# Kernel tuning notes

Hardware: AMD Instinct MI355X
Metric: run time of the kernel (lower is better)

The kernel has to match this reference:

```python
import jax, jax.numpy as jnp
import numpy as np

B, S, D, H = 2, 2048, 1024, 16
DK = D // H


def setup_inputs() -> dict:
    key = jax.random.key(0)
    ks = jax.random.split(key, 12)
    scale = 1.0 / np.sqrt(D)
    return {
        "query": jax.random.normal(ks[0], (B, S, D), jnp.float32),
        "key": jax.random.normal(ks[1], (B, S, D), jnp.float32),
        "value": jax.random.normal(ks[2], (B, S, D), jnp.float32),
        "mask": jax.random.randint(ks[3], (B, S), 0, 2, jnp.int32),
        "Wq": jax.random.normal(ks[4], (D, D), jnp.float32) * scale,
        "bq": jnp.zeros((D,), jnp.float32),
        "Wk": jax.random.normal(ks[5], (D, D), jnp.float32) * scale,
        "bk": jnp.zeros((D,), jnp.float32),
        "Wv": jax.random.normal(ks[6], (D, D), jnp.float32) * scale,
        "bv": jnp.zeros((D,), jnp.float32),
        "Wo": jax.random.normal(ks[7], (D, D), jnp.float32) * scale,
        "bo": jnp.zeros((D,), jnp.float32),
    }


def _proj_split(x, W, b):
    # torch Linear: x @ W.T + b, then [B,S,D] -> [B,H,S,DK]
    y = x @ W.T + b
    return y.reshape(B, S, H, DK).transpose(0, 2, 1, 3)


def reference(query, key, value, mask, Wq, bq, Wk, bk, Wv, bv, Wo, bo):
    q = _proj_split(query, Wq, bq)  # [B,H,S,DK]
    k = _proj_split(key, Wk, bk)
    v = _proj_split(value, Wv, bv)
    scores = jnp.einsum("bhqd,bhkd->bhqk", q, k) / jnp.sqrt(jnp.float32(DK))
    # 2D mask -> [B,1,1,S], masked_fill(mask==0, -1e9)
    m = mask[:, None, None, :]
    scores = jnp.where(m == 0, jnp.float32(-1e9), scores)
    attn = jax.nn.softmax(scores, axis=-1)  # dropout p=0.0 -> identity
    x = jnp.einsum("bhqk,bhkd->bhqd", attn, v)
    x = x.transpose(0, 2, 1, 3).reshape(B, S, D)
    output = x @ Wo.T + bo
    return output, attn
```

## Files before the change

kernel.cpp:

```cpp
#include <hip/hip_runtime.h>
#include <hip/hip_bf16.h>
#include <stdint.h>

typedef __bf16 bf16;
typedef __bf16 bf16x8 __attribute__((ext_vector_type(8)));
typedef float f32x4 __attribute__((ext_vector_type(4)));

#define MFMA16(a, b, c) __builtin_amdgcn_mfma_f32_16x16x32_bf16((a), (b), (c), 0, 0, 0)

__device__ __forceinline__ void g2lds16(const void* g, void* l) {
  __builtin_amdgcn_global_load_lds((__attribute__((address_space(1))) void*)g,
                                   (__attribute__((address_space(3))) void*)l,
                                   16, 0, 0);
}

__global__ __launch_bounds__(256) void cvt3(const float* __restrict__ a,
                                            const float* __restrict__ b,
                                            const float* __restrict__ c,
                                            bf16* x, bf16* y, bf16* z_) {
  int zi = blockIdx.y;
  const float* s = (zi == 0) ? a : (zi == 1) ? b : c;
  bf16* d = (zi == 0) ? x : (zi == 1) ? y : z_;
  size_t i = ((size_t)blockIdx.x * 256 + threadIdx.x) * 8;
  float4 f0 = *(const float4*)(s + i);
  float4 f1 = *(const float4*)(s + i + 4);
  union { bf16 h[8]; uint4 u; } t;
  t.h[0] = (bf16)f0.x; t.h[1] = (bf16)f0.y; t.h[2] = (bf16)f0.z; t.h[3] = (bf16)f0.w;
  t.h[4] = (bf16)f1.x; t.h[5] = (bf16)f1.y; t.h[6] = (bf16)f1.z; t.h[7] = (bf16)f1.w;
  *(uint4*)(d + i) = t.u;
}
__global__ __launch_bounds__(256) void cvt4(const float* __restrict__ a,
                                            const float* __restrict__ b,
                                            const float* __restrict__ c,
                                            const float* __restrict__ e,
                                            bf16* x, bf16* y, bf16* z_, bf16* w) {
  int zi = blockIdx.y;
  const float* s = (zi == 0) ? a : (zi == 1) ? b : (zi == 2) ? c : e;
  bf16* d = (zi == 0) ? x : (zi == 1) ? y : (zi == 2) ? z_ : w;
  size_t i = ((size_t)blockIdx.x * 256 + threadIdx.x) * 8;
  float4 f0 = *(const float4*)(s + i);
  float4 f1 = *(const float4*)(s + i + 4);
  union { bf16 h[8]; uint4 u; } t;
  t.h[0] = (bf16)f0.x; t.h[1] = (bf16)f0.y; t.h[2] = (bf16)f0.z; t.h[3] = (bf16)f0.w;
  t.h[4] = (bf16)f1.x; t.h[5] = (bf16)f1.y; t.h[6] = (bf16)f1.z; t.h[7] = (bf16)f1.w;
  *(uint4*)(d + i) = t.u;
}

__device__ __forceinline__ void gemm_core_128(const bf16* __restrict__ A,
                                              const bf16* __restrict__ W,
                                              int m0, int n0, int tid,
                                              uint4* sA, uint4* sB,
                                              f32x4 acc[4][4]) {
  const int lane = tid & 63, quad = lane >> 4, l16 = lane & 15;
  const int wave = tid >> 6;
  const int wm = (wave >> 1) * 64, wn = (wave & 1) * 64;
#pragma unroll
  for (int i = 0; i < 4; i++)
#pragma unroll
    for (int j = 0; j < 4; j++) {
      f32x4 z = {0.f, 0.f, 0.f, 0.f};
      acc[i][j] = z;
    }
  for (int kk = 0; kk < 16; kk++) {
    const int k0 = kk * 64;
    __syncthreads();
#pragma unroll
    for (int t = 0; t < 4; t++) {
      int c = t * 256 + tid;
      int r = c >> 3, jb = (c & 7) ^ (r & 7);
      g2lds16(A + (size_t)(m0 + r) * 1024 + k0 + jb * 8, sA + c);
    }
#pragma unroll
    for (int t = 0; t < 4; t++) {
      int c = t * 256 + tid;
      int r = c >> 3, jb = (c & 7) ^ (r & 7);
      g2lds16(W + (size_t)(n0 + r) * 1024 + k0 + jb * 8, sB + c);
    }
    __syncthreads();
#pragma unroll
    for (int kc = 0; kc < 2; kc++) {
      bf16x8 af[4], bfr[4];
#pragma unroll
      for (int i = 0; i < 4; i++) {
        int row = wm + i * 16 + l16;
        af[i] = *(const bf16x8*)(sA + row * 8 + (((kc << 2) + quad) ^ (row & 7)));
      }
#pragma unroll
      for (int j = 0; j < 4; j++) {
        int row = wn + j * 16 + l16;
        bfr[j] = *(const bf16x8*)(sB + row * 8 + (((kc << 2) + quad) ^ (row & 7)));
      }
#pragma unroll
      for (int i = 0; i < 4; i++)
#pragma unroll
        for (int j = 0; j < 4; j++)
          acc[i][j] = MFMA16(af[i], bfr[j], acc[i][j]);
    }
  }
}


__global__ __launch_bounds__(256, 3) void qkv_gemm(
    const bf16* __restrict__ qin, const bf16* __restrict__ kin,
    const bf16* __restrict__ vin, const bf16* __restrict__ Wq,
    const bf16* __restrict__ Wk, const bf16* __restrict__ Wv,
    const float* __restrict__ bq, const float* __restrict__ bk,
    const float* __restrict__ bv, bf16* __restrict__ qw, bf16* __restrict__ kw,
    bf16* __restrict__ vTw) {
  __shared__ uint4 sA[1024], sB[1024];
  const int z = blockIdx.z;
  const bf16* A = (z == 0) ? qin : (z == 1) ? kin : vin;
  const bf16* W = (z == 0) ? Wq : (z == 1) ? Wk : Wv;
  const float* bias = (z == 0) ? bq : (z == 1) ? bk : bv;
  const int m0 = blockIdx.x * 128, n0 = blockIdx.y * 128;
  const int tid = threadIdx.x;
  f32x4 acc[4][4];
  gemm_core_128(A, W, m0, n0, tid, sA, sB, acc);
  const int lane = tid & 63, quad = lane >> 4, l16 = lane & 15;
  const int wave = tid >> 6;
  const int wm = (wave >> 1) * 64, wn = (wave & 1) * 64;
  if (z < 2) {
    bf16* out = (z == 0) ? qw : kw;
#pragma unroll
    for (int j = 0; j < 4; j++) {
      int n = n0 + wn + j * 16 + l16;
      float bvv = bias[n];
      int h = n >> 6, dk = n & 63;
#pragma unroll
      for (int i = 0; i < 4; i++) {
        int mbase = m0 + wm + i * 16 + quad * 4;
#pragma unroll
        for (int r = 0; r < 4; r++) {
          int m = mbase + r;
          int b = m >> 11, s = m & 2047;
          out[(((size_t)(b * 16 + h) * 2048 + s) << 6) + dk] =
              (bf16)(acc[i][j][r] + bvv);
        }
      }
    }
  } else {
#pragma unroll
    for (int j = 0; j < 4; j++) {
      int n = n0 + wn + j * 16 + l16;
      float bvv = bias[n];
      int h = n >> 6, dk = n & 63;
#pragma unroll
      for (int i = 0; i < 4; i++) {
        int m = m0 + wm + i * 16 + quad * 4;
        int b = m >> 11, s = m & 2047;
        union { bf16 hh[4]; uint2 u; } tmp;
#pragma unroll
        for (int r = 0; r < 4; r++) tmp.hh[r] = (bf16)(acc[i][j][r] + bvv);
        *(uint2*)&vTw[((size_t)((b * 16 + h) * 64 + dk) << 11) + s] = tmp.u;
      }
    }
  }
}

__global__ __launch_bounds__(256, 3) void out_gemm(const bf16* __restrict__ X,
                                                   const bf16* __restrict__ Wo,
                                                   const float* __restrict__ bo,
                                                   float* __restrict__ out) {
  __shared__ uint4 sA[1024], sB[1024];
  const int m0 = blockIdx.x * 128, n0 = blockIdx.y * 128;
  const int tid = threadIdx.x;
  f32x4 acc[4][4];
  gemm_core_128(X, Wo, m0, n0, tid, sA, sB, acc);
  const int lane = tid & 63, quad = lane >> 4, l16 = lane & 15;
  const int wave = tid >> 6;
  const int wm = (wave >> 1) * 64, wn = (wave & 1) * 64;
#pragma unroll
  for (int j = 0; j < 4; j++) {
    int n = n0 + wn + j * 16 + l16;
    float bvv = bo[n];
#pragma unroll
    for (int i = 0; i < 4; i++) {
      int mbase = m0 + wm + i * 16 + quad * 4;
#pragma unroll
      for (int r = 0; r < 4; r++) {
        int m = mbase + r;
        out[((size_t)m << 10) + n] = acc[i][j][r] + bvv;
      }
    }
  }
}

__global__ __launch_bounds__(256, 2) void attn_kernel(
    const bf16* __restrict__ qw, const bf16* __restrict__ kw,
    const bf16* __restrict__ vT, const int* __restrict__ mask,
    float* __restrict__ attnF, bf16* __restrict__ xw) {
  __shared__ uint4 smem[4096];
  uint4* const sK0 = smem;
  uint4* const sK1 = smem + 1024;
  uint4* const sV = smem + 2048;
  uint4* const sP = smem + 3072;
  uint4* const sQ = smem + 3072;

  const int tid = threadIdx.x, wave = tid >> 6, lane = tid & 63;
  const int quad = lane >> 4, l16 = lane & 15;
  const int wgid = blockIdx.y * 32 + blockIdx.x;
  const int swz = (wgid & 7) * 128 + (wgid >> 3);
  const int qt = swz & 31, bh = swz >> 5, b = bh >> 4, h = bh & 15;
  const int q0 = qt * 64;
  const bf16* qbase = qw + (size_t)bh * (2048 * 64);
  const bf16* kbase = kw + (size_t)bh * (2048 * 64);
  const bf16* vbase = vT + (size_t)bh * (64 * 2048);
  const int* mrow = mask + b * 2048;

  const float SC = 0.125f * 1.44269504f;

  auto stageK = [&](uint4* buf, int kt) {
#pragma unroll
    for (int t = 0; t < 4; t++) {
      int c = t * 256 + tid;
      int r = c >> 3, jb = (c & 7) ^ (r & 7);
      g2lds16(kbase + (size_t)(kt * 128 + r) * 64 + jb * 8, buf + c);
    }
  };
  auto stageV = [&](int kt) {
#pragma unroll
    for (int t = 0; t < 4; t++) {
      int c = t * 256 + tid;
      int rv = c >> 4, jb = (c & 15) ^ (rv & 15);
      g2lds16(vbase + (size_t)rv * 2048 + kt * 128 + jb * 8, sV + c);
    }
  };

#pragma unroll
  for (int t = 0; t < 2; t++) {
    int c = t * 256 + tid;
    int r = c >> 3, jb = (c & 7) ^ (r & 7);
    g2lds16(qbase + (size_t)(q0 + r) * 64 + jb * 8, sQ + c);
  }
  stageK(sK0, 0);
  __syncthreads();

  bf16x8 aq[2];
  {
    int row = wave * 16 + l16;
    aq[0] = *(const bf16x8*)(sQ + row * 8 + ((quad) ^ (row & 7)));
    aq[1] = *(const bf16x8*)(sQ + row * 8 + ((4 + quad) ^ (row & 7)));
  }
  float lpart[4];
#pragma unroll
  for (int r = 0; r < 4; r++) lpart[r] = 0.f;

  for (int kt = 0; kt < 16; kt++) {
    uint4* kcur = (kt & 1) ? sK1 : sK0;
    if (kt < 15) {
      stageK((kt & 1) ? sK0 : sK1, kt + 1);
    } else {
      stageK(sK0, 0);
      stageV(0);
    }
    f32x4 sc[8];
#pragma unroll
    for (int ns = 0; ns < 8; ns++) {
      f32x4 z = {0.f, 0.f, 0.f, 0.f};
      sc[ns] = z;
    }
#pragma unroll
    for (int kc = 0; kc < 2; kc++)
#pragma unroll
      for (int ns = 0; ns < 8; ns++) {
        int row = ns * 16 + l16;
        bf16x8 bk =
            *(const bf16x8*)(kcur + row * 8 + (((kc << 2) + quad) ^ (row & 7)));
        sc[ns] = MFMA16(aq[kc], bk, sc[ns]);
      }
#pragma unroll
    for (int ns = 0; ns < 8; ns++) {
      float madd = (mrow[kt * 128 + ns * 16 + l16] == 0) ? -1.0e9f : 0.0f;
#pragma unroll
      for (int r = 0; r < 4; r++)
        lpart[r] += exp2f(sc[ns][r] * SC + madd);
    }
    __syncthreads();
  }

  float invl[4];
  size_t arow[4];
#pragma unroll
  for (int r = 0; r < 4; r++) {
    float v = lpart[r];
#pragma unroll
    for (int off = 8; off >= 1; off >>= 1) v += __shfl_xor(v, off, 16);
    invl[r] = 1.f / fmaxf(v, 1.0e-30f);
    arow[r] = (size_t)(bh * 2048 + q0 + wave * 16 + quad * 4 + r) * 2048;
  }
  f32x4 xacc[4];
#pragma unroll
  for (int nd = 0; nd < 4; nd++) {
    f32x4 z = {0.f, 0.f, 0.f, 0.f};
    xacc[nd] = z;
  }
  bf16* sPb = (bf16*)sP;

  for (int kt = 0; kt < 16; kt++) {
    uint4* kcur = (kt & 1) ? sK1 : sK0;
    if (kt < 15) stageK((kt & 1) ? sK0 : sK1, kt + 1);
    f32x4 sc[8];
#pragma unroll
    for (int ns = 0; ns < 8; ns++) {
      f32x4 z = {0.f, 0.f, 0.f, 0.f};
      sc[ns] = z;
    }
#pragma unroll
    for (int kc = 0; kc < 2; kc++)
#pragma unroll
      for (int ns = 0; ns < 8; ns++) {
        int row = ns * 16 + l16;
        bf16x8 bk =
            *(const bf16x8*)(kcur + row * 8 + (((kc << 2) + quad) ^ (row & 7)));
        sc[ns] = MFMA16(aq[kc], bk, sc[ns]);
      }
#pragma unroll
    for (int ns = 0; ns < 8; ns++) {
      float madd = (mrow[kt * 128 + ns * 16 + l16] == 0) ? -1.0e9f : 0.0f;
      int col = ns * 16 + l16;
#pragma unroll
      for (int r = 0; r < 4; r++) {
        float p = exp2f(sc[ns][r] * SC + madd) * invl[r];
        sc[ns][r] = p;
        int qrow = wave * 16 + quad * 4 + r;
        int chunk = qrow * 16 + ((col >> 3) ^ (qrow & 15));
        sPb[chunk * 8 + (col & 7)] = (bf16)p;
      }
    }
    __syncthreads();
#pragma unroll
    for (int kc2 = 0; kc2 < 4; kc2++) {
      int rowp = wave * 16 + l16;
      bf16x8 ap =
          *(const bf16x8*)(sP + rowp * 16 + (((kc2 << 2) + quad) ^ (rowp & 15)));
#pragma unroll
      for (int nd = 0; nd < 4; nd++) {
        int rv = nd * 16 + l16;
        bf16x8 bv =
            *(const bf16x8*)(sV + rv * 16 + (((kc2 << 2) + quad) ^ (rv & 15)));
        xacc[nd] = MFMA16(ap, bv, xacc[nd]);
      }
    }
    __syncthreads();
    if (kt < 15) stageV(kt + 1);
#pragma unroll
    for (int ns = 0; ns < 8; ns++) {
      int col = kt * 128 + ns * 16 + l16;
#pragma unroll
      for (int r = 0; r < 4; r++)
        __builtin_nontemporal_store(sc[ns][r], &attnF[arow[r] + col]);
    }
  }
#pragma unroll
  for (int nd = 0; nd < 4; nd++) {
    int dk = nd * 16 + l16;
#pragma unroll
    for (int r = 0; r < 4; r++) {
      int qrow = q0 + wave * 16 + quad * 4 + r;
      xw[((size_t)(b * 2048 + qrow) << 10) + h * 64 + dk] = (bf16)xacc[nd][r];
    }
  }
}

extern "C" void kernel_launch(void* const* d_in, const int* in_sizes, int n_in,
                              void* d_out, int out_size, void* d_ws,
                              size_t ws_size, hipStream_t stream) {
  const float* query = (const float*)d_in[0];
  const float* key = (const float*)d_in[1];
  const float* value = (const float*)d_in[2];
  const int* mask = (const int*)d_in[3];
  const float* Wq = (const float*)d_in[4];
  const float* bq = (const float*)d_in[5];
  const float* Wk = (const float*)d_in[6];
  const float* bk = (const float*)d_in[7];
  const float* Wv = (const float*)d_in[8];
  const float* bv = (const float*)d_in[9];
  const float* Wo = (const float*)d_in[10];
  const float* bo = (const float*)d_in[11];

  float* outF = (float*)d_out;
  float* attnF = outF + (size_t)4194304;

  bf16* tQ = (bf16*)attnF;
  bf16* tK = tQ + (size_t)4194304;
  bf16* tV = tK + (size_t)4194304;
  bf16* tWq = tV + (size_t)4194304;
  bf16* tWk = tWq + (size_t)1048576;
  bf16* tWv = tWk + (size_t)1048576;

  bf16* qw = (bf16*)d_ws;
  bf16* kw = qw + (size_t)4194304;
  bf16* vT = kw + (size_t)4194304;
  bf16* xw = vT + (size_t)4194304;
  bf16* WoB = xw + (size_t)4194304;

  cvt3<<<dim3(2048, 3), 256, 0, stream>>>(query, key, value, tQ, tK, tV);
  cvt4<<<dim3(512, 4), 256, 0, stream>>>(Wq, Wk, Wv, Wo, tWq, tWk, tWv, WoB);
  qkv_gemm<<<dim3(32, 8, 3), 256, 0, stream>>>(tQ, tK, tV, tWq, tWk, tWv, bq,
                                               bk, bv, qw, kw, vT);
  attn_kernel<<<dim3(32, 32), 256, 0, stream>>>(qw, kw, vT, mask, attnF, xw);
  out_gemm<<<dim3(32, 8), 256, 0, stream>>>(xw, WoB, bo, outF);
}
```

Baseline: 725.5 us.

## Double attention query tile to 128 rows per workgroup for K/V reuse

Each workgroup now handles 128 query rows instead of 64, so each wave processes two 16-row subtiles against every staged K and V tile. Each K/V tile loaded into shared memory is reused twice as much, which halves K/V global traffic and staging work, and the grid is halved. In exchange, register pressure roughly doubles for scores and accumulators, shared memory grows, and there are fewer workgroups to fill the GPU.

```diff
diff --git a/kernel.cpp b/kernel.cpp
--- a/kernel.cpp
+++ b/kernel.cpp
@@ -189,7 +189,7 @@
     const bf16* __restrict__ qw, const bf16* __restrict__ kw,
     const bf16* __restrict__ vT, const int* __restrict__ mask,
     float* __restrict__ attnF, bf16* __restrict__ xw) {
-  __shared__ uint4 smem[4096];
+  __shared__ uint4 smem[5120];
   uint4* const sK0 = smem;
   uint4* const sK1 = smem + 1024;
   uint4* const sV = smem + 2048;
@@ -198,10 +198,10 @@
 
   const int tid = threadIdx.x, wave = tid >> 6, lane = tid & 63;
   const int quad = lane >> 4, l16 = lane & 15;
-  const int wgid = blockIdx.y * 32 + blockIdx.x;
-  const int swz = (wgid & 7) * 128 + (wgid >> 3);
-  const int qt = swz & 31, bh = swz >> 5, b = bh >> 4, h = bh & 15;
-  const int q0 = qt * 64;
+  const int wgid = blockIdx.y * 16 + blockIdx.x;
+  const int swz = (wgid & 7) * 64 + (wgid >> 3);
+  const int qt = swz & 15, bh = swz >> 4, b = bh >> 4, h = bh & 15;
+  const int q0 = qt * 128;
   const bf16* qbase = qw + (size_t)bh * (2048 * 64);
   const bf16* kbase = kw + (size_t)bh * (2048 * 64);
   const bf16* vbase = vT + (size_t)bh * (64 * 2048);
@@ -227,7 +227,7 @@
   };
 
 #pragma unroll
-  for (int t = 0; t < 2; t++) {
+  for (int t = 0; t < 4; t++) {
     int c = t * 256 + tid;
     int r = c >> 3, jb = (c & 7) ^ (r & 7);
     g2lds16(qbase + (size_t)(q0 + r) * 64 + jb * 8, sQ + c);
@@ -235,15 +235,18 @@
   stageK(sK0, 0);
   __syncthreads();
 
-  bf16x8 aq[2];
-  {
-    int row = wave * 16 + l16;
-    aq[0] = *(const bf16x8*)(sQ + row * 8 + ((quad) ^ (row & 7)));
-    aq[1] = *(const bf16x8*)(sQ + row * 8 + ((4 + quad) ^ (row & 7)));
-  }
-  float lpart[4];
-#pragma unroll
-  for (int r = 0; r < 4; r++) lpart[r] = 0.f;
+  bf16x8 aq[2][2];
+#pragma unroll
+  for (int st = 0; st < 2; st++) {
+    int row = wave * 32 + st * 16 + l16;
+    aq[st][0] = *(const bf16x8*)(sQ + row * 8 + ((quad) ^ (row & 7)));
+    aq[st][1] = *(const bf16x8*)(sQ + row * 8 + ((4 + quad) ^ (row & 7)));
+  }
+  float lpart[2][4];
+#pragma unroll
+  for (int st = 0; st < 2; st++)
+#pragma unroll
+    for (int r = 0; r < 4; r++) lpart[st][r] = 0.f;
 
   for (int kt = 0; kt < 16; kt++) {
     uint4* kcur = (kt & 1) ? sK1 : sK0;
@@ -253,113 +256,134 @@
       stageK(sK0, 0);
       stageV(0);
     }
-    f32x4 sc[8];
-#pragma unroll
-    for (int ns = 0; ns < 8; ns++) {
+#pragma unroll
+    for (int st = 0; st < 2; st++) {
+      f32x4 sc[8];
+#pragma unroll
+      for (int ns = 0; ns < 8; ns++) {
+        f32x4 z = {0.f, 0.f, 0.f, 0.f};
+        sc[ns] = z;
+      }
+#pragma unroll
+      for (int kc = 0; kc < 2; kc++)
+#pragma unroll
+        for (int ns = 0; ns < 8; ns++) {
+          int row = ns * 16 + l16;
+          bf16x8 bk = *(const bf16x8*)(kcur + row * 8 +
+                                       (((kc << 2) + quad) ^ (row & 7)));
+          sc[ns] = MFMA16(aq[st][kc], bk, sc[ns]);
+        }
+#pragma unroll
+      for (int ns = 0; ns < 8; ns++) {
+        float madd = (mrow[kt * 128 + ns * 16 + l16] == 0) ? -1.0e9f : 0.0f;
+#pragma unroll
+        for (int r = 0; r < 4; r++)
+          lpart[st][r] += exp2f(sc[ns][r] * SC + madd);
+      }
+    }
+    __syncthreads();
+  }
+
+  float invl[2][4];
+  size_t arow[2][4];
+#pragma unroll
+  for (int st = 0; st < 2; st++)
+#pragma unroll
+    for (int r = 0; r < 4; r++) {
+      float v = lpart[st][r];
+#pragma unroll
+      for (int off = 8; off >= 1; off >>= 1) v += __shfl_xor(v, off, 16);
+      invl[st][r] = 1.f / fmaxf(v, 1.0e-30f);
+      arow[st][r] =
+          (size_t)(bh * 2048 + q0 + wave * 32 + st * 16 + quad * 4 + r) * 2048;
+    }
+  f32x4 xacc[2][4];
+#pragma unroll
+  for (int st = 0; st < 2; st++)
+#pragma unroll
+    for (int nd = 0; nd < 4; nd++) {
       f32x4 z = {0.f, 0.f, 0.f, 0.f};
-      sc[ns] = z;
-    }
-#pragma unroll
-    for (int kc = 0; kc < 2; kc++)
-#pragma unroll
-      for (int ns = 0; ns < 8; ns++) {
-        int row = ns * 16 + l16;
-        bf16x8 bk =
-            *(const bf16x8*)(kcur + row * 8 + (((kc << 2) + quad) ^ (row & 7)));
-        sc[ns] = MFMA16(aq[kc], bk, sc[ns]);
-      }
-#pragma unroll
-    for (int ns = 0; ns < 8; ns++) {
-      float madd = (mrow[kt * 128 + ns * 16 + l16] == 0) ? -1.0e9f : 0.0f;
-#pragma unroll
-      for (int r = 0; r < 4; r++)
-        lpart[r] += exp2f(sc[ns][r] * SC + madd);
-    }
-    __syncthreads();
-  }
-
-  float invl[4];
-  size_t arow[4];
-#pragma unroll
-  for (int r = 0; r < 4; r++) {
-    float v = lpart[r];
-#pragma unroll
-    for (int off = 8; off >= 1; off >>= 1) v += __shfl_xor(v, off, 16);
-    invl[r] = 1.f / fmaxf(v, 1.0e-30f);
-    arow[r] = (size_t)(bh * 2048 + q0 + wave * 16 + quad * 4 + r) * 2048;
-  }
-  f32x4 xacc[4];
-#pragma unroll
-  for (int nd = 0; nd < 4; nd++) {
-    f32x4 z = {0.f, 0.f, 0.f, 0.f};
-    xacc[nd] = z;
-  }
+      xacc[st][nd] = z;
+    }
   bf16* sPb = (bf16*)sP;
 
   for (int kt = 0; kt < 16; kt++) {
     uint4* kcur = (kt & 1) ? sK1 : sK0;
     if (kt < 15) stageK((kt & 1) ? sK0 : sK1, kt + 1);
-    f32x4 sc[8];
-#pragma unroll
-    for (int ns = 0; ns < 8; ns++) {
-      f32x4 z = {0.f, 0.f, 0.f, 0.f};
-      sc[ns] = z;
-    }
-#pragma unroll
-    for (int kc = 0; kc < 2; kc++)
+    f32x4 sc[2][8];
+#pragma unroll
+    for (int st = 0; st < 2; st++)
 #pragma unroll
       for (int ns = 0; ns < 8; ns++) {
-        int row = ns * 16 + l16;
-        bf16x8 bk =
-            *(const bf16x8*)(kcur + row * 8 + (((kc << 2) + quad) ^ (row & 7)));
-        sc[ns] = MFMA16(aq[kc], bk, sc[ns]);
-      }
-#pragma unroll
-    for (int ns = 0; ns < 8; ns++) {
-      float madd = (mrow[kt * 128 + ns * 16 + l16] == 0) ? -1.0e9f : 0.0f;
-      int col = ns * 16 + l16;
-#pragma unroll
-      for (int r = 0; r < 4; r++) {
-        float p = exp2f(sc[ns][r] * SC + madd) * invl[r];
-        sc[ns][r] = p;
-        int qrow = wave * 16 + quad * 4 + r;
-        int chunk = qrow * 16 + ((col >> 3) ^ (qrow & 15));
-        sPb[chunk * 8 + (col & 7)] = (bf16)p;
-      }
-    }
+        f32x4 z = {0.f, 0.f, 0.f, 0.f};
+        sc[st][ns] = z;
+      }
+#pragma unroll
+    for (int st = 0; st < 2; st++)
+#pragma unroll
+      for (int kc = 0; kc < 2; kc++)
+#pragma unroll
+        for (int ns = 0; ns < 8; ns++) {
+          int row = ns * 16 + l16;
+          bf16x8 bk = *(const bf16x8*)(kcur + row * 8 +
+                                       (((kc << 2) + quad) ^ (row & 7)));
+          sc[st][ns] = MFMA16(aq[st][kc], bk, sc[st][ns]);
+        }
+#pragma unroll
+    for (int st = 0; st < 2; st++)
+#pragma unroll
+      for (int ns = 0; ns < 8; ns++) {
+        float madd = (mrow[kt * 128 + ns * 16 + l16] == 0) ? -1.0e9f : 0.0f;
+        int col = ns * 16 + l16;
+#pragma unroll
+        for (int r = 0; r < 4; r++) {
+          float p = exp2f(sc[st][ns][r] * SC + madd) * invl[st][r];
+          sc[st][ns][r] = p;
+          int qrow = wave * 32 + st * 16 + quad * 4 + r;
+          int chunk = qrow * 16 + ((col >> 3) ^ (qrow & 15));
+          sPb[chunk * 8 + (col & 7)] = (bf16)p;
+        }
+      }
     __syncthreads();
 #pragma unroll
-    for (int kc2 = 0; kc2 < 4; kc2++) {
-      int rowp = wave * 16 + l16;
-      bf16x8 ap =
-          *(const bf16x8*)(sP + rowp * 16 + (((kc2 << 2) + quad) ^ (rowp & 15)));
-#pragma unroll
-      for (int nd = 0; nd < 4; nd++) {
-        int rv = nd * 16 + l16;
-        bf16x8 bv =
-            *(const bf16x8*)(sV + rv * 16 + (((kc2 << 2) + quad) ^ (rv & 15)));
-        xacc[nd] = MFMA16(ap, bv, xacc[nd]);
-      }
-    }
+    for (int st = 0; st < 2; st++)
+#pragma unroll
+      for (int kc2 = 0; kc2 < 4; kc2++) {
+        int rowp = wave * 32 + st * 16 + l16;
+        bf16x8 ap = *(const bf16x8*)(sP + rowp * 16 +
+                                     (((kc2 << 2) + quad) ^ (rowp & 15)));
+#pragma unroll
+        for (int nd = 0; nd < 4; nd++) {
+          int rv = nd * 16 + l16;
+          bf16x8 bv = *(const bf16x8*)(sV + rv * 16 +
+                                       (((kc2 << 2) + quad) ^ (rv & 15)));
+          xacc[st][nd] = MFMA16(ap, bv, xacc[st][nd]);
+        }
+      }
     __syncthreads();
     if (kt < 15) stageV(kt + 1);
 #pragma unroll
-    for (int ns = 0; ns < 8; ns++) {
-      int col = kt * 128 + ns * 16 + l16;
-#pragma unroll
-      for (int r = 0; r < 4; r++)
-        __builtin_nontemporal_store(sc[ns][r], &attnF[arow[r] + col]);
-    }
-  }
-#pragma unroll
-  for (int nd = 0; nd < 4; nd++) {
-    int dk = nd * 16 + l16;
-#pragma unroll
-    for (int r = 0; r < 4; r++) {
-      int qrow = q0 + wave * 16 + quad * 4 + r;
-      xw[((size_t)(b * 2048 + qrow) << 10) + h * 64 + dk] = (bf16)xacc[nd][r];
-    }
-  }
+    for (int st = 0; st < 2; st++)
+#pragma unroll
+      for (int ns = 0; ns < 8; ns++) {
+        int col = kt * 128 + ns * 16 + l16;
+#pragma unroll
+        for (int r = 0; r < 4; r++)
+          __builtin_nontemporal_store(sc[st][ns][r], &attnF[arow[st][r] + col]);
+      }
+  }
+#pragma unroll
+  for (int st = 0; st < 2; st++)
+#pragma unroll
+    for (int nd = 0; nd < 4; nd++) {
+      int dk = nd * 16 + l16;
+#pragma unroll
+      for (int r = 0; r < 4; r++) {
+        int qrow = q0 + wave * 32 + st * 16 + quad * 4 + r;
+        xw[((size_t)(b * 2048 + qrow) << 10) + h * 64 + dk] =
+            (bf16)xacc[st][nd][r];
+      }
+    }
 }
 
 extern "C" void kernel_launch(void* const* d_in, const int* in_sizes, int n_in,
@@ -398,6 +422,6 @@
   cvt4<<<dim3(512, 4), 256, 0, stream>>>(Wq, Wk, Wv, Wo, tWq, tWk, tWv, WoB);
   qkv_gemm<<<dim3(32, 8, 3), 256, 0, stream>>>(tQ, tK, tV, tWq, tWk, tWv, bq,
                                                bk, bv, qw, kw, vT);
-  attn_kernel<<<dim3(32, 32), 256, 0, stream>>>(qw, kw, vT, mask, attnF, xw);
+  attn_kernel<<<dim3(16, 32), 256, 0, stream>>>(qw, kw, vT, mask, attnF, xw);
   out_gemm<<<dim3(32, 8), 256, 0, stream>>>(xw, WoB, bo, outF);
 }
```

Measured after the change: 756.2 us. 4.2% more time.
